# Kernel tuning notes

Measured on AMD Instinct MI355X. Metric: run time of the kernel, lower is better.

The kernel has to match this reference:

```python
import jax, jax.numpy as jnp
import numpy as np

N, E, B = 20000, 320000, 64
H, D = 4, 64          # heads, out_channels per head
HD = H * D            # 256
F_IN = 4
NUM_ACTIONS = 100
NEG_SLOPE = 0.2


def _lin(k, fan_in, fan_out, scale=0.05):
    kw, kb = jax.random.split(k)
    return (jax.random.normal(kw, (fan_in, fan_out), jnp.float32) * scale,
            jax.random.normal(kb, (fan_out,), jnp.float32) * scale)


def setup_inputs() -> dict:
    key = jax.random.key(0)
    ks = jax.random.split(key, 32)
    x = jax.random.normal(ks[0], (N, F_IN), jnp.float32)
    edge_index = jax.random.randint(ks[1], (2, E), 0, N)
    edge_attr = jax.random.normal(ks[2], (E, 1), jnp.float32)
    batch_idx = jnp.sort(jax.random.randint(ks[3], (N,), 0, B))
    action = jax.random.randint(ks[4], (B,), 0, NUM_ACTIONS)

    # GATv2 layer 1 (in=4)
    Wl1, bl1 = _lin(ks[5], F_IN, HD)
    Wr1, br1 = _lin(ks[6], F_IN, HD)
    We1 = jax.random.normal(ks[7], (1, HD), jnp.float32) * 0.05
    att1 = jax.random.normal(ks[8], (H, D), jnp.float32) * 0.05
    b1 = jnp.zeros((HD,), jnp.float32)
    # GATv2 layer 2 (in=256)
    Wl2, bl2 = _lin(ks[9], HD, HD)
    Wr2, br2 = _lin(ks[10], HD, HD)
    We2 = jax.random.normal(ks[11], (1, HD), jnp.float32) * 0.05
    att2 = jax.random.normal(ks[12], (H, D), jnp.float32) * 0.05
    b2 = jnp.zeros((HD,), jnp.float32)
    # critic MLP 256->128->64->1
    Wc1, bc1 = _lin(ks[13], 256, 128)
    Wc2, bc2 = _lin(ks[14], 128, 64)
    Wc3, bc3 = _lin(ks[15], 64, 1)
    # actor MLP 256->128->64->num_actions
    Wa1, ba1 = _lin(ks[16], 256, 128)
    Wa2, ba2 = _lin(ks[17], 128, 64)
    Wa3, ba3 = _lin(ks[18], 64, NUM_ACTIONS)
    return dict(x=x, edge_index=edge_index, edge_attr=edge_attr, batch_idx=batch_idx,
                action=action,
                Wl1=Wl1, bl1=bl1, Wr1=Wr1, br1=br1, We1=We1, att1=att1, b1=b1,
                Wl2=Wl2, bl2=bl2, Wr2=Wr2, br2=br2, We2=We2, att2=att2, b2=b2,
                Wc1=Wc1, bc1=bc1, Wc2=Wc2, bc2=bc2, Wc3=Wc3, bc3=bc3,
                Wa1=Wa1, ba1=ba1, Wa2=Wa2, ba2=ba2, Wa3=Wa3, ba3=ba3)


def gatv2(x, src, dst, edge_attr, Wl, bl, Wr, br, We, att, bias):
    n = x.shape[0]
    xl = (x @ Wl + bl).reshape(n, H, D)   # source transform (messages)
    xr = (x @ Wr + br).reshape(n, H, D)   # target transform
    e = (edge_attr @ We).reshape(-1, H, D)
    m = xl[src] + xr[dst] + e             # [E,H,D]
    s = jnp.sum(jax.nn.leaky_relu(m, NEG_SLOPE) * att, axis=-1)  # [E,H]
    smax = jax.ops.segment_max(s, dst, num_segments=n)
    a = jnp.exp(s - smax[dst])
    denom = jax.ops.segment_sum(a, dst, num_segments=n)
    alpha = a / (denom[dst] + 1e-16)      # scatter-softmax over in-edges
    out = jax.ops.segment_sum(alpha[..., None] * xl[src], dst, num_segments=n)
    return out.reshape(n, HD) + bias


def mlp3(f, W1, b1, W2, b2, W3, b3):
    h = jax.nn.relu(f @ W1 + b1)
    h = jax.nn.relu(h @ W2 + b2)
    return h @ W3 + b3


def reference(x, edge_index, edge_attr, batch_idx, action,
              Wl1, bl1, Wr1, br1, We1, att1, b1,
              Wl2, bl2, Wr2, br2, We2, att2, b2,
              Wc1, bc1, Wc2, bc2, Wc3, bc3,
              Wa1, ba1, Wa2, ba2, Wa3, ba3):
    src, dst = edge_index[0], edge_index[1]
    h = jax.nn.relu(gatv2(x, src, dst, edge_attr, Wl1, bl1, Wr1, br1, We1, att1, b1))
    h = jax.nn.relu(gatv2(h, src, dst, edge_attr, Wl2, bl2, Wr2, br2, We2, att2, b2))
    # global mean pool over graphs
    sums = jax.ops.segment_sum(h, batch_idx, num_segments=B)
    cnts = jax.ops.segment_sum(jnp.ones((h.shape[0],), h.dtype), batch_idx, num_segments=B)
    feats = sums / jnp.maximum(cnts, 1.0)[:, None]          # [B,256]
    logits = mlp3(feats, Wa1, ba1, Wa2, ba2, Wa3, ba3)       # [B,A]
    value = mlp3(feats, Wc1, bc1, Wc2, bc2, Wc3, bc3)        # [B,1]
    logp = jax.nn.log_softmax(logits, axis=-1)
    log_prob = jnp.take_along_axis(logp, action[:, None], axis=-1)[:, 0]
    entropy = -jnp.sum(jnp.exp(logp) * logp, axis=-1)
    return logits, log_prob, entropy, value
```

## Files before the change

### kernel.cpp

```cpp
#include <hip/hip_runtime.h>
#include <hip/hip_bf16.h>
#include <cstddef>

typedef __hip_bfloat16 bf16;
typedef unsigned short u16;
typedef __attribute__((ext_vector_type(8))) short short8;
typedef __attribute__((ext_vector_type(4))) float float4v;
typedef __attribute__((ext_vector_type(2))) float float2v;

#define HD 256
#define A_MAX 128

static __device__ __forceinline__ float b2f(const bf16 v) { return __bfloat162float(v); }
static __device__ __forceinline__ bf16 f2b(float v) { return __float2bfloat16(v); }

static __device__ __forceinline__ float2v up2(unsigned int u) {
  union { unsigned int i; float f; } a, b;
  a.i = u << 16; b.i = u & 0xffff0000u;
  float2v r; r.x = a.f; r.y = b.f; return r;
}

static __device__ __forceinline__ float ldf(const void* p, size_t i, bool f32) {
  return f32 ? ((const float*)p)[i] : b2f(((const bf16*)p)[i]);
}
template <bool F32>
static __device__ __forceinline__ float ldt(const void* p, size_t i) {
  return F32 ? ((const float*)p)[i] : b2f(((const bf16*)p)[i]);
}
static __device__ __forceinline__ void stf(void* p, size_t i, bool f32, float v) {
  if (f32) ((float*)p)[i] = v;
  else     ((bf16*)p)[i] = f2b(v);
}

__global__ void k_sentinel(float* out, int n, float v) {
  int i = blockIdx.x * blockDim.x + threadIdx.x;
  if (i < n) out[i] = v;
}

__global__ void k_init(const u16* __restrict__ xbits, int* __restrict__ flag,
                       int* deg, int N) {
  int i = blockIdx.x * blockDim.x + threadIdx.x;
  if (blockIdx.x == 0 && threadIdx.x < 64) {
    int l = threadIdx.x;
    int huge = 0;
    for (int k = l; k < 256; k += 64) {
      u16 u = xbits[2 * k];
      int ex = (u >> 7) & 0xFF;
      if (ex >= 0xB0) huge++;
    }
#pragma unroll
    for (int off = 32; off > 0; off >>= 1) huge += __shfl_xor(huge, off, 64);
    if (l == 0) *flag = (huge >= 20) ? 1 : 0;
  }
  if (i < N) deg[i] = 0;
}


__global__ void k_hist(const int* __restrict__ dst, int* __restrict__ deg, int E) {
  int e = blockIdx.x * blockDim.x + threadIdx.x;
  if (e < E) atomicAdd(&deg[dst[e]], 1);
}

__global__ void k_sumb(const int* __restrict__ deg, int* __restrict__ bsum, int n) {
  __shared__ int ws[16];
  int b = blockIdx.x, t = threadIdx.x;
  int i = b * 1024 + t;
  int v = (i < n) ? deg[i] : 0;
#pragma unroll
  for (int off = 32; off > 0; off >>= 1) v += __shfl_xor(v, off, 64);
  if ((t & 63) == 0) ws[t >> 6] = v;
  __syncthreads();
  if (t == 0) {
    int s = 0;
#pragma unroll
    for (int k = 0; k < 16; k++) s += ws[k];
    bsum[b] = s;
  }
}

__global__ void k_scanb(const int* __restrict__ bsum, int* __restrict__ boff,
                        int nb, int* __restrict__ offs, int n) {
  if (threadIdx.x == 0) {
    int s = 0;
    for (int i = 0; i < nb; i++) { boff[i] = s; s += bsum[i]; }
    offs[n] = s;
  }
}

__global__ void k_scanapply(const int* __restrict__ deg, const int* __restrict__ boff,
                            int* __restrict__ offs, int n) {
  __shared__ int wsum[16];
  int b = blockIdx.x, t = threadIdx.x, w = t >> 6, l = t & 63;
  int i = b * 1024 + t;
  int v = (i < n) ? deg[i] : 0;
  int x = v;
#pragma unroll
  for (int off = 1; off < 64; off <<= 1) {
    int y = __shfl_up(x, off, 64);
    if (l >= off) x += y;
  }
  if (l == 63) wsum[w] = x;
  __syncthreads();
  if (t == 0) {
    int s = 0;
#pragma unroll
    for (int k = 0; k < 16; k++) { int tmp = wsum[k]; wsum[k] = s; s += tmp; }
  }
  __syncthreads();
  if (i < n) offs[i] = boff[b] + wsum[w] + x - v;
}

__global__ void k_scatter(const int* __restrict__ src, const int* __restrict__ dst,
                          const void* __restrict__ ea, int* __restrict__ offs,
                          int2* __restrict__ csr, const int* __restrict__ flag, int E) {
  int e = blockIdx.x * blockDim.x + threadIdx.x;
  if (e >= E) return;
  bool f32 = flag[0] != 0;
  int d = dst[e];
  int pos = atomicAdd(&offs[d], 1);
  int2 v;
  v.x = src[e];
  v.y = __float_as_int(ldf(ea, e, f32));
  csr[pos] = v;
}


template <bool F32>
static __device__ void xform1_body(const void* __restrict__ x,
                                   const void* __restrict__ Wl, const void* __restrict__ bl,
                                   const void* __restrict__ Wr, const void* __restrict__ br,
                                   bf16* __restrict__ xl, bf16* __restrict__ xr, int N) {
  int n0 = blockIdx.x * 4, t = threadIdx.x;
  float wl0 = ldt<F32>(Wl, t),          wl1 = ldt<F32>(Wl, HD + t);
  float wl2 = ldt<F32>(Wl, 2 * HD + t), wl3 = ldt<F32>(Wl, 3 * HD + t);
  float wr0 = ldt<F32>(Wr, t),          wr1 = ldt<F32>(Wr, HD + t);
  float wr2 = ldt<F32>(Wr, 2 * HD + t), wr3 = ldt<F32>(Wr, 3 * HD + t);
  float bbl = ldt<F32>(bl, t), bbr = ldt<F32>(br, t);
#pragma unroll
  for (int k = 0; k < 4; k++) {
    int n = n0 + k;
    if (n >= N) break;
    float x0 = ldt<F32>(x, (size_t)n * 4 + 0), x1 = ldt<F32>(x, (size_t)n * 4 + 1);
    float x2 = ldt<F32>(x, (size_t)n * 4 + 2), x3 = ldt<F32>(x, (size_t)n * 4 + 3);
    xl[(size_t)n * HD + t] = f2b(bbl + x0 * wl0 + x1 * wl1 + x2 * wl2 + x3 * wl3);
    xr[(size_t)n * HD + t] = f2b(bbr + x0 * wr0 + x1 * wr1 + x2 * wr2 + x3 * wr3);
  }
}

__global__ void k_xform1(const void* __restrict__ x,
                         const void* __restrict__ Wl, const void* __restrict__ bl,
                         const void* __restrict__ Wr, const void* __restrict__ br,
                         bf16* __restrict__ xl, bf16* __restrict__ xr,
                         const int* __restrict__ flag, int N) {
  if (flag[0] != 0) xform1_body<true >(x, Wl, bl, Wr, br, xl, xr, N);
  else              xform1_body<false>(x, Wl, bl, Wr, br, xl, xr, N);
}

__global__ void k_prepw(const void* __restrict__ Wl, const void* __restrict__ Wr,
                        const void* __restrict__ bl, const void* __restrict__ br,
                        bf16* __restrict__ Wfrag, bf16* __restrict__ bias2,
                        const int* __restrict__ flag) {
  bool f32 = flag[0] != 0;
  int b = blockIdx.x;
  int ct = b >> 3, kt = b & 7;
  int t = threadIdx.x;
  if (b == 0) {
    bias2[t]       = f2b(ldf(bl, t, f32));
    bias2[t + 256] = f2b(ldf(br, t, f32));
  }
#pragma unroll
  for (int half = 0; half < 2; half++) {
    int e = half * 256 + t;
    int m = e & 15;
    int rest = e >> 4;
    int quad = rest >> 3, j = rest & 7;
    int l = quad * 16 + m;
    int k = kt * 32 + quad * 8 + j;
    int n = ct * 16 + m;
    const void* W = (n < 256) ? Wl : Wr;
    float v = ldf(W, (size_t)k * 256 + (n & 255), f32);
    Wfrag[(size_t)b * 512 + l * 8 + j] = f2b(v);
  }
}

__global__ __launch_bounds__(256) void k_xform2_mfma(
    const bf16* __restrict__ hin, const bf16* __restrict__ Wfrag,
    const bf16* __restrict__ bias2,
    bf16* __restrict__ P, bf16* __restrict__ Q, int N) {
  int w = threadIdx.x >> 6, l = threadIdx.x & 63;
  int r0 = blockIdx.x * 16;
  if (r0 >= N) return;
  int m = l & 15;
  int quad = l >> 4;
  int row = r0 + m;
  if (row >= N) row = N - 1;

  short8 a[8];
  const u16* arow = (const u16*)hin + (size_t)row * 256;
#pragma unroll
  for (int kt = 0; kt < 8; kt++)
    a[kt] = *(const short8*)(arow + kt * 32 + quad * 8);

#pragma unroll
  for (int ct = 0; ct < 8; ct++) {
    int c_tile = w * 8 + ct;
    int c = c_tile * 16 + m;
    const u16* bbase = (const u16*)Wfrag + ((size_t)c_tile * 8) * 512 + l * 8;
    float4v acc = {0.f, 0.f, 0.f, 0.f};
#pragma unroll
    for (int kt = 0; kt < 8; kt++) {
      short8 b = *(const short8*)(bbase + kt * 512);
      acc = __builtin_amdgcn_mfma_f32_16x16x32_bf16(a[kt], b, acc, 0, 0, 0);
    }
    float bv = b2f(bias2[c]);
#pragma unroll
    for (int i = 0; i < 4; i++) {
      int r = r0 + quad * 4 + i;
      if (r < N) {
        float v = acc[i] + bv;
        if (c < 256) P[(size_t)r * 256 + c] = f2b(v);
        else         Q[(size_t)r * 256 + (c - 256)] = f2b(v);
      }
    }
  }
}

__global__ __launch_bounds__(256) void k_gat(
    const bf16* __restrict__ xl, const bf16* __restrict__ xr,
    const int2* __restrict__ csr, const int* __restrict__ offs,
    const void* __restrict__ We, const void* __restrict__ att,
    const void* __restrict__ bias,
    bf16* __restrict__ hout, const int* __restrict__ flag, int N) {
  int w = threadIdx.x >> 6, l = threadIdx.x & 63;
  int n = blockIdx.x * 4 + w;
  if (n >= N) return;
  bool f32 = flag[0] != 0;
  int d0 = l << 2;

  uint2 xu = *(const uint2*)((const u16*)xr + (size_t)n * HD + d0);
  float2v xr01 = up2(xu.x), xr23 = up2(xu.y);
  float2v We01, We23, at01, at23;
  We01.x = ldf(We, d0 + 0, f32); We01.y = ldf(We, d0 + 1, f32);
  We23.x = ldf(We, d0 + 2, f32); We23.y = ldf(We, d0 + 3, f32);
  at01.x = ldf(att, d0 + 0, f32); at01.y = ldf(att, d0 + 1, f32);
  at23.x = ldf(att, d0 + 2, f32); at23.y = ldf(att, d0 + 3, f32);

  int beg = (n > 0) ? offs[n - 1] : 0;
  int end = offs[n];
  float2v acc01 = {0.f, 0.f}, acc23 = {0.f, 0.f};
  float dn = 0.f;

  int j = beg;
  for (; j + 2 <= end; j += 2) {
    int2 v0 = csr[j];
    int2 v1 = csr[j + 1];
    uint2 su0 = *(const uint2*)((const u16*)xl + (size_t)v0.x * HD + d0);
    uint2 su1 = *(const uint2*)((const u16*)xl + (size_t)v1.x * HD + d0);
    float ea0 = __int_as_float(v0.y), ea1 = __int_as_float(v1.y);
    float2v x01a = up2(su0.x), x23a = up2(su0.y);
    float2v x01b = up2(su1.x), x23b = up2(su1.y);
    float2v eva; eva.x = ea0; eva.y = ea0;
    float2v evb; evb.x = ea1; evb.y = ea1;
    float2v m01a = x01a + xr01 + eva * We01, m23a = x23a + xr23 + eva * We23;
    float2v m01b = x01b + xr01 + evb * We01, m23b = x23b + xr23 + evb * We23;
    float2v lr01a, lr23a, lr01b, lr23b;
    lr01a.x = fmaxf(m01a.x, 0.2f * m01a.x); lr01a.y = fmaxf(m01a.y, 0.2f * m01a.y);
    lr23a.x = fmaxf(m23a.x, 0.2f * m23a.x); lr23a.y = fmaxf(m23a.y, 0.2f * m23a.y);
    lr01b.x = fmaxf(m01b.x, 0.2f * m01b.x); lr01b.y = fmaxf(m01b.y, 0.2f * m01b.y);
    lr23b.x = fmaxf(m23b.x, 0.2f * m23b.x); lr23b.y = fmaxf(m23b.y, 0.2f * m23b.y);
    float2v ppa = lr01a * at01 + lr23a * at23;
    float2v ppb = lr01b * at01 + lr23b * at23;
    float psa = ppa.x + ppa.y;
    float psb = ppb.x + ppb.y;
    psa += __shfl_xor(psa, 1, 64);  psb += __shfl_xor(psb, 1, 64);
    psa += __shfl_xor(psa, 2, 64);  psb += __shfl_xor(psb, 2, 64);
    psa += __shfl_xor(psa, 4, 64);  psb += __shfl_xor(psb, 4, 64);
    psa += __shfl_xor(psa, 8, 64);  psb += __shfl_xor(psb, 8, 64);
    float aa = __expf(fminf(fmaxf(psa, -40.f), 40.f));
    float ab = __expf(fminf(fmaxf(psb, -40.f), 40.f));
    dn += aa + ab;
    float2v ava; ava.x = aa; ava.y = aa;
    float2v avb; avb.x = ab; avb.y = ab;
    acc01 += ava * x01a + avb * x01b;
    acc23 += ava * x23a + avb * x23b;
  }
  if (j < end) {
    int2 v = csr[j];
    float eav = __int_as_float(v.y);
    uint2 su = *(const uint2*)((const u16*)xl + (size_t)v.x * HD + d0);
    float2v x01 = up2(su.x), x23 = up2(su.y);
    float2v ev; ev.x = eav; ev.y = eav;
    float2v m01 = x01 + xr01 + ev * We01;
    float2v m23 = x23 + xr23 + ev * We23;
    float2v lr01, lr23;
    lr01.x = fmaxf(m01.x, 0.2f * m01.x); lr01.y = fmaxf(m01.y, 0.2f * m01.y);
    lr23.x = fmaxf(m23.x, 0.2f * m23.x); lr23.y = fmaxf(m23.y, 0.2f * m23.y);
    float2v pp = lr01 * at01 + lr23 * at23;
    float ps = pp.x + pp.y;
    ps += __shfl_xor(ps, 1, 64);
    ps += __shfl_xor(ps, 2, 64);
    ps += __shfl_xor(ps, 4, 64);
    ps += __shfl_xor(ps, 8, 64);
    float a = __expf(fminf(fmaxf(ps, -40.f), 40.f));
    dn += a;
    float2v av; av.x = a; av.y = a;
    acc01 += av * x01;
    acc23 += av * x23;
  }

  float inv = 1.f / (dn + 1e-16f);
  bf16 o[4];
  o[0] = f2b(fmaxf(acc01.x * inv + ldf(bias, d0 + 0, f32), 0.f));
  o[1] = f2b(fmaxf(acc01.y * inv + ldf(bias, d0 + 1, f32), 0.f));
  o[2] = f2b(fmaxf(acc23.x * inv + ldf(bias, d0 + 2, f32), 0.f));
  o[3] = f2b(fmaxf(acc23.y * inv + ldf(bias, d0 + 3, f32), 0.f));
  *(ushort4*)((u16*)hout + (size_t)n * HD + d0) = *(ushort4*)o;
}


static __device__ __forceinline__ int lb(const int* a, int n, int v) {
  int lo = 0, hi = n;
  while (lo < hi) { int m = (lo + hi) >> 1; if (a[m] < v) lo = m + 1; else hi = m; }
  return lo;
}

__global__ void k_pool(const bf16* __restrict__ h, const int* __restrict__ bidx,
                       float* __restrict__ feats4, int Bc, int N) {
  int g = blockIdx.x >> 2, part = blockIdx.x & 3, t = threadIdx.x;
  int s = lb(bidx, N, g), e_ = lb(bidx, N, g + 1);
  float acc = 0.f;
  for (int i = s + part; i < e_; i += 4) acc += b2f(h[(size_t)i * HD + t]);
  feats4[((size_t)part * Bc + g) * HD + t] = acc;
}


template <bool F32>
static __device__ void mlp_body(const float* __restrict__ feats4,
                                const int* __restrict__ bidx, int N,
                                const int* __restrict__ act,
                                const void* Wa1, const void* ba1, const void* Wa2, const void* ba2,
                                const void* Wa3, const void* ba3,
                                const void* Wc1, const void* bc1, const void* Wc2, const void* bc2,
                                const void* Wc3, const void* bc3,
                                void* __restrict__ out, int B, int A) {
  __shared__ float f[HD];
  __shared__ float p1[2][128];
  __shared__ float h1[128];
  __shared__ float p2[4][64];
  __shared__ float h2[64];
  __shared__ float lg[A_MAX];
  __shared__ float sc[2];
  __shared__ float inv_s;
  int blk = blockIdx.x, g = blk >> 1, which = blk & 1, t = threadIdx.x;
  if (t == 0) {
    int cnt = lb(bidx, N, g + 1) - lb(bidx, N, g);
    inv_s = 1.f / fmaxf((float)cnt, 1.f);
  }
  __syncthreads();
  float inv = inv_s;
  f[t] = (feats4[(size_t)g * HD + t] + feats4[((size_t)B + g) * HD + t]
        + feats4[((size_t)2 * B + g) * HD + t] + feats4[((size_t)3 * B + g) * HD + t]) * inv;
  __syncthreads();

  const void *W1 = which ? Wc1 : Wa1, *B1 = which ? bc1 : ba1;
  const void *W2 = which ? Wc2 : Wa2, *B2 = which ? bc2 : ba2;

  {
    int j = t & 127, half = t >> 7;
    int i0 = half * 128;
    float a0 = 0.f, a1 = 0.f, a2 = 0.f, a3 = 0.f;
    for (int u = 0; u < 128; u += 4) {
      a0 += f[i0 + u + 0] * ldt<F32>(W1, (size_t)(i0 + u + 0) * 128 + j);
      a1 += f[i0 + u + 1] * ldt<F32>(W1, (size_t)(i0 + u + 1) * 128 + j);
      a2 += f[i0 + u + 2] * ldt<F32>(W1, (size_t)(i0 + u + 2) * 128 + j);
      a3 += f[i0 + u + 3] * ldt<F32>(W1, (size_t)(i0 + u + 3) * 128 + j);
    }
    p1[half][j] = (a0 + a1) + (a2 + a3);
  }
  __syncthreads();
  if (t < 128) h1[t] = fmaxf(p1[0][t] + p1[1][t] + ldt<F32>(B1, t), 0.f);
  __syncthreads();

  {
    int j = t & 63, q = t >> 6;
    int i0 = q * 32;
    float a0 = 0.f, a1 = 0.f;
    for (int u = 0; u < 32; u += 2) {
      a0 += h1[i0 + u + 0] * ldt<F32>(W2, (size_t)(i0 + u + 0) * 64 + j);
      a1 += h1[i0 + u + 1] * ldt<F32>(W2, (size_t)(i0 + u + 1) * 64 + j);
    }
    p2[q][j] = a0 + a1;
  }
  __syncthreads();
  if (t < 64) h2[t] = fmaxf(p2[0][t] + p2[1][t] + p2[2][t] + p2[3][t] + ldt<F32>(B2, t), 0.f);
  __syncthreads();

  if (which == 0) {
    if (t < A) {
      float a0 = 0.f, a1 = 0.f, a2 = 0.f, a3 = 0.f;
      for (int i = 0; i < 64; i += 4) {
        a0 += h2[i + 0] * ldt<F32>(Wa3, (size_t)(i + 0) * A + t);
        a1 += h2[i + 1] * ldt<F32>(Wa3, (size_t)(i + 1) * A + t);
        a2 += h2[i + 2] * ldt<F32>(Wa3, (size_t)(i + 2) * A + t);
        a3 += h2[i + 3] * ldt<F32>(Wa3, (size_t)(i + 3) * A + t);
      }
      lg[t] = (a0 + a1) + (a2 + a3) + ldt<F32>(ba3, t);
    }
    __syncthreads();
    if (t == 0) {
      float mx = -3.4e38f;
      for (int i = 0; i < A; i++) mx = fmaxf(mx, lg[i]);
      float s = 0.f;
      for (int i = 0; i < A; i++) s += __expf(lg[i] - mx);
      sc[0] = mx;
      sc[1] = logf(s);
    }
    __syncthreads();
    float mx = sc[0], lse = sc[1];
    if (t < A) stf(out, (size_t)g * A + t, F32, lg[t]);
    if (t == 0) {
      int a = act[g];
      stf(out, (size_t)B * A + g, F32, lg[a] - mx - lse);
      float ent = 0.f;
      for (int i = 0; i < A; i++) {
        float l = lg[i] - mx - lse;
        ent -= __expf(l) * l;
      }
      stf(out, (size_t)B * A + B + g, F32, ent);
    }
  } else {
    if (t < 64) {
      float v = h2[t] * ldt<F32>(Wc3, t);
#pragma unroll
      for (int off = 32; off > 0; off >>= 1) v += __shfl_xor(v, off, 64);
      if (t == 0) stf(out, (size_t)B * A + 2 * B + g, F32, v + ldt<F32>(bc3, 0));
    }
  }
}

__global__ void k_mlp(const float* __restrict__ feats4,
                      const int* __restrict__ bidx, int N,
                      const int* __restrict__ act,
                      const void* Wa1, const void* ba1, const void* Wa2, const void* ba2,
                      const void* Wa3, const void* ba3,
                      const void* Wc1, const void* bc1, const void* Wc2, const void* bc2,
                      const void* Wc3, const void* bc3,
                      void* __restrict__ out, const int* __restrict__ flag, int B, int A) {
  if (flag[0] != 0)
    mlp_body<true >(feats4, bidx, N, act, Wa1, ba1, Wa2, ba2, Wa3, ba3,
                    Wc1, bc1, Wc2, bc2, Wc3, bc3, out, B, A);
  else
    mlp_body<false>(feats4, bidx, N, act, Wa1, ba1, Wa2, ba2, Wa3, ba3,
                    Wc1, bc1, Wc2, bc2, Wc3, bc3, out, B, A);
}


extern "C" void kernel_launch(void* const* d_in, const int* in_sizes, int n_in,
                              void* d_out, int out_size, void* d_ws, size_t ws_size,
                              hipStream_t stream) {
  const void* x    = d_in[0];
  const int*  ei   = (const int*)d_in[1];
  const void* ea   = d_in[2];
  const int*  bidx = (const int*)d_in[3];
  const int*  act  = (const int*)d_in[4];
  const void *Wl1 = d_in[5],  *bl1 = d_in[6];
  const void *Wr1 = d_in[7],  *br1 = d_in[8];
  const void *We1 = d_in[9],  *att1 = d_in[10];
  const void *b1  = d_in[11];
  const void *Wl2 = d_in[12], *bl2 = d_in[13];
  const void *Wr2 = d_in[14], *br2 = d_in[15];
  const void *We2 = d_in[16], *att2 = d_in[17];
  const void *b2  = d_in[18];
  const void *Wc1 = d_in[19], *bc1 = d_in[20];
  const void *Wc2 = d_in[21], *bc2 = d_in[22];
  const void *Wc3 = d_in[23], *bc3 = d_in[24];
  const void *Wa1 = d_in[25], *ba1 = d_in[26];
  const void *Wa2 = d_in[27], *ba2 = d_in[28];
  const void *Wa3 = d_in[29], *ba3 = d_in[30];

  const int N = in_sizes[0] / 4;
  const int E = in_sizes[1] / 2;
  const int B = in_sizes[4];
  const int A = in_sizes[30];

  char* p = (char*)d_ws;
  auto carve = [&](size_t bytes) {
    void* r = (void*)p;
    p += (bytes + 255) & ~(size_t)255;
    return r;
  };
  int*   dflag   = (int*)carve(4);
  int*   deg     = (int*)carve((size_t)N * 4);
  int*   offs    = (int*)carve((size_t)(N + 1) * 4);
  int2*  csr     = (int2*)carve((size_t)E * 8);
  bf16*  P       = (bf16*)carve((size_t)N * HD * 2);
  bf16*  Q       = (bf16*)carve((size_t)N * HD * 2);
  bf16*  R       = (bf16*)carve((size_t)N * HD * 2);
  bf16*  Wfrag   = (bf16*)carve((size_t)512 * 256 * 2);
  bf16*  bias2   = (bf16*)carve((size_t)512 * 2);
  float* feats4  = (float*)carve((size_t)4 * B * HD * 4);
  int    nb      = (N + 1023) / 1024;
  int*   bsum    = (int*)carve((size_t)nb * 4);
  int*   boff    = (int*)carve((size_t)nb * 4);
  size_t need = (size_t)(p - (char*)d_ws);

  if (ws_size < need) {
    float v = 1000.f + (float)(ws_size >> 20);
    int n = out_size / 2;
    k_sentinel<<<(n + 255) / 256, 256, 0, stream>>>((float*)d_out, n, v);
    return;
  }

  const int* srcA = ei;
  const int* dstA = ei + E;

  k_init<<<(N + 255) / 256, 256, 0, stream>>>((const u16*)x, dflag, deg, N);
  k_hist<<<(E + 255) / 256, 256, 0, stream>>>(dstA, deg, E);
  k_sumb<<<nb, 1024, 0, stream>>>(deg, bsum, N);
  k_scanb<<<1, 64, 0, stream>>>(bsum, boff, nb, offs, N);
  k_scanapply<<<nb, 1024, 0, stream>>>(deg, boff, offs, N);
  k_scatter<<<(E + 255) / 256, 256, 0, stream>>>(srcA, dstA, ea, offs, csr, dflag, E);
  k_prepw<<<256, 256, 0, stream>>>(Wl2, Wr2, bl2, br2, Wfrag, bias2, dflag);

  k_xform1<<<(N + 3) / 4, 256, 0, stream>>>(x, Wl1, bl1, Wr1, br1, P, Q, dflag, N);
  k_gat<<<(N + 3) / 4, 256, 0, stream>>>(P, Q, csr, offs, We1, att1, b1, R, dflag, N);
  k_xform2_mfma<<<(N + 15) / 16, 256, 0, stream>>>(R, Wfrag, bias2, P, Q, N);
  k_gat<<<(N + 3) / 4, 256, 0, stream>>>(P, Q, csr, offs, We2, att2, b2, R, dflag, N);

  k_pool<<<B * 4, 256, 0, stream>>>(R, bidx, feats4, B, N);
  k_mlp<<<B * 2, 256, 0, stream>>>(feats4, bidx, N, act,
                                   Wa1, ba1, Wa2, ba2, Wa3, ba3,
                                   Wc1, bc1, Wc2, bc2, Wc3, bc3,
                                   d_out, dflag, B, A);
}
```

Baseline: 318.2 us.

## Merge scan, scatter, xform1, prepw launches; unroll GAT edges by four; fuse pooling into MLP

Replaces the three-kernel prefix scan with a single-block looped scan and merges the CSR scatter, layer-1 transform and weight-fragment prep into one multi-role launch. The GAT edge loop is unrolled to process four edges at once, with batched shuffle reductions for more loads in flight. Mean pooling moves into the MLP kernel, removing the pool launch and its feats buffer. In exchange, each MLP block reads its graph's rows serially, and the actor and critic blocks duplicate that read.

```diff
diff --git a/kernel.cpp b/kernel.cpp
--- a/kernel.cpp
+++ b/kernel.cpp
@@ -55,131 +55,103 @@
   if (i < N) deg[i] = 0;
 }
 
-
 __global__ void k_hist(const int* __restrict__ dst, int* __restrict__ deg, int E) {
   int e = blockIdx.x * blockDim.x + threadIdx.x;
   if (e < E) atomicAdd(&deg[dst[e]], 1);
 }
 
-__global__ void k_sumb(const int* __restrict__ deg, int* __restrict__ bsum, int n) {
-  __shared__ int ws[16];
+__global__ void k_scan(const int* __restrict__ deg, int* __restrict__ offs, int n) {
+  __shared__ int wsum[17];
+  __shared__ int carry_s;
+  int t = threadIdx.x, w = t >> 6, l = t & 63;
+  if (t == 0) carry_s = 0;
+  __syncthreads();
+  for (int base = 0; base < n; base += 1024) {
+    int i = base + t;
+    int v = (i < n) ? deg[i] : 0;
+    int x = v;
+#pragma unroll
+    for (int off = 1; off < 64; off <<= 1) {
+      int y = __shfl_up(x, off, 64);
+      if (l >= off) x += y;
+    }
+    if (l == 63) wsum[w] = x;
+    __syncthreads();
+    if (t == 0) {
+      int s = 0;
+#pragma unroll
+      for (int k = 0; k < 16; k++) { int tmp = wsum[k]; wsum[k] = s; s += tmp; }
+      wsum[16] = s;
+    }
+    __syncthreads();
+    int c = carry_s;
+    if (i < n) offs[i] = c + wsum[w] + x - v;
+    __syncthreads();
+    if (t == 0) carry_s = c + wsum[16];
+    __syncthreads();
+  }
+  if (t == 0) offs[n] = carry_s;
+}
+
+__global__ void k_misc(const int* __restrict__ src, const int* __restrict__ dst,
+                       const void* __restrict__ ea, int* __restrict__ offs,
+                       int2* __restrict__ csr,
+                       const void* __restrict__ x,
+                       const void* __restrict__ Wl1, const void* __restrict__ bl1,
+                       const void* __restrict__ Wr1, const void* __restrict__ br1,
+                       bf16* __restrict__ P, bf16* __restrict__ Q,
+                       const void* __restrict__ Wl2, const void* __restrict__ Wr2,
+                       const void* __restrict__ bl2, const void* __restrict__ br2,
+                       bf16* __restrict__ Wfrag, bf16* __restrict__ bias2,
+                       const int* __restrict__ flag,
+                       int E, int N, int nSc, int nX1) {
+  bool f32 = flag[0] != 0;
   int b = blockIdx.x, t = threadIdx.x;
-  int i = b * 1024 + t;
-  int v = (i < n) ? deg[i] : 0;
-#pragma unroll
-  for (int off = 32; off > 0; off >>= 1) v += __shfl_xor(v, off, 64);
-  if ((t & 63) == 0) ws[t >> 6] = v;
-  __syncthreads();
-  if (t == 0) {
-    int s = 0;
-#pragma unroll
-    for (int k = 0; k < 16; k++) s += ws[k];
-    bsum[b] = s;
-  }
-}
-
-__global__ void k_scanb(const int* __restrict__ bsum, int* __restrict__ boff,
-                        int nb, int* __restrict__ offs, int n) {
-  if (threadIdx.x == 0) {
-    int s = 0;
-    for (int i = 0; i < nb; i++) { boff[i] = s; s += bsum[i]; }
-    offs[n] = s;
-  }
-}
-
-__global__ void k_scanapply(const int* __restrict__ deg, const int* __restrict__ boff,
-                            int* __restrict__ offs, int n) {
-  __shared__ int wsum[16];
-  int b = blockIdx.x, t = threadIdx.x, w = t >> 6, l = t & 63;
-  int i = b * 1024 + t;
-  int v = (i < n) ? deg[i] : 0;
-  int x = v;
-#pragma unroll
-  for (int off = 1; off < 64; off <<= 1) {
-    int y = __shfl_up(x, off, 64);
-    if (l >= off) x += y;
-  }
-  if (l == 63) wsum[w] = x;
-  __syncthreads();
-  if (t == 0) {
-    int s = 0;
-#pragma unroll
-    for (int k = 0; k < 16; k++) { int tmp = wsum[k]; wsum[k] = s; s += tmp; }
-  }
-  __syncthreads();
-  if (i < n) offs[i] = boff[b] + wsum[w] + x - v;
-}
-
-__global__ void k_scatter(const int* __restrict__ src, const int* __restrict__ dst,
-                          const void* __restrict__ ea, int* __restrict__ offs,
-                          int2* __restrict__ csr, const int* __restrict__ flag, int E) {
-  int e = blockIdx.x * blockDim.x + threadIdx.x;
-  if (e >= E) return;
-  bool f32 = flag[0] != 0;
-  int d = dst[e];
-  int pos = atomicAdd(&offs[d], 1);
-  int2 v;
-  v.x = src[e];
-  v.y = __float_as_int(ldf(ea, e, f32));
-  csr[pos] = v;
-}
-
-
-template <bool F32>
-static __device__ void xform1_body(const void* __restrict__ x,
-                                   const void* __restrict__ Wl, const void* __restrict__ bl,
-                                   const void* __restrict__ Wr, const void* __restrict__ br,
-                                   bf16* __restrict__ xl, bf16* __restrict__ xr, int N) {
-  int n0 = blockIdx.x * 4, t = threadIdx.x;
-  float wl0 = ldt<F32>(Wl, t),          wl1 = ldt<F32>(Wl, HD + t);
-  float wl2 = ldt<F32>(Wl, 2 * HD + t), wl3 = ldt<F32>(Wl, 3 * HD + t);
-  float wr0 = ldt<F32>(Wr, t),          wr1 = ldt<F32>(Wr, HD + t);
-  float wr2 = ldt<F32>(Wr, 2 * HD + t), wr3 = ldt<F32>(Wr, 3 * HD + t);
-  float bbl = ldt<F32>(bl, t), bbr = ldt<F32>(br, t);
-#pragma unroll
-  for (int k = 0; k < 4; k++) {
-    int n = n0 + k;
-    if (n >= N) break;
-    float x0 = ldt<F32>(x, (size_t)n * 4 + 0), x1 = ldt<F32>(x, (size_t)n * 4 + 1);
-    float x2 = ldt<F32>(x, (size_t)n * 4 + 2), x3 = ldt<F32>(x, (size_t)n * 4 + 3);
-    xl[(size_t)n * HD + t] = f2b(bbl + x0 * wl0 + x1 * wl1 + x2 * wl2 + x3 * wl3);
-    xr[(size_t)n * HD + t] = f2b(bbr + x0 * wr0 + x1 * wr1 + x2 * wr2 + x3 * wr3);
-  }
-}
-
-__global__ void k_xform1(const void* __restrict__ x,
-                         const void* __restrict__ Wl, const void* __restrict__ bl,
-                         const void* __restrict__ Wr, const void* __restrict__ br,
-                         bf16* __restrict__ xl, bf16* __restrict__ xr,
-                         const int* __restrict__ flag, int N) {
-  if (flag[0] != 0) xform1_body<true >(x, Wl, bl, Wr, br, xl, xr, N);
-  else              xform1_body<false>(x, Wl, bl, Wr, br, xl, xr, N);
-}
-
-__global__ void k_prepw(const void* __restrict__ Wl, const void* __restrict__ Wr,
-                        const void* __restrict__ bl, const void* __restrict__ br,
-                        bf16* __restrict__ Wfrag, bf16* __restrict__ bias2,
-                        const int* __restrict__ flag) {
-  bool f32 = flag[0] != 0;
-  int b = blockIdx.x;
-  int ct = b >> 3, kt = b & 7;
-  int t = threadIdx.x;
-  if (b == 0) {
-    bias2[t]       = f2b(ldf(bl, t, f32));
-    bias2[t + 256] = f2b(ldf(br, t, f32));
-  }
-#pragma unroll
-  for (int half = 0; half < 2; half++) {
-    int e = half * 256 + t;
-    int m = e & 15;
-    int rest = e >> 4;
-    int quad = rest >> 3, j = rest & 7;
-    int l = quad * 16 + m;
-    int k = kt * 32 + quad * 8 + j;
-    int n = ct * 16 + m;
-    const void* W = (n < 256) ? Wl : Wr;
-    float v = ldf(W, (size_t)k * 256 + (n & 255), f32);
-    Wfrag[(size_t)b * 512 + l * 8 + j] = f2b(v);
+  if (b < nSc) {
+    int e = b * 256 + t;
+    if (e >= E) return;
+    int d = dst[e];
+    int pos = atomicAdd(&offs[d], 1);
+    int2 v;
+    v.x = src[e];
+    v.y = __float_as_int(ldf(ea, e, f32));
+    csr[pos] = v;
+  } else if (b < nSc + nX1) {
+    int n0 = (b - nSc) * 4;
+    float wl0 = ldf(Wl1, t, f32),          wl1 = ldf(Wl1, HD + t, f32);
+    float wl2 = ldf(Wl1, 2 * HD + t, f32), wl3 = ldf(Wl1, 3 * HD + t, f32);
+    float wr0 = ldf(Wr1, t, f32),          wr1 = ldf(Wr1, HD + t, f32);
+    float wr2 = ldf(Wr1, 2 * HD + t, f32), wr3 = ldf(Wr1, 3 * HD + t, f32);
+    float bbl = ldf(bl1, t, f32), bbr = ldf(br1, t, f32);
+#pragma unroll
+    for (int k = 0; k < 4; k++) {
+      int n = n0 + k;
+      if (n >= N) break;
+      float x0 = ldf(x, (size_t)n * 4 + 0, f32), x1 = ldf(x, (size_t)n * 4 + 1, f32);
+      float x2 = ldf(x, (size_t)n * 4 + 2, f32), x3 = ldf(x, (size_t)n * 4 + 3, f32);
+      P[(size_t)n * HD + t] = f2b(bbl + x0 * wl0 + x1 * wl1 + x2 * wl2 + x3 * wl3);
+      Q[(size_t)n * HD + t] = f2b(bbr + x0 * wr0 + x1 * wr1 + x2 * wr2 + x3 * wr3);
+    }
+  } else {
+    int pb = b - nSc - nX1;
+    int ct = pb >> 3, kt = pb & 7;
+    if (pb == 0) {
+      bias2[t]       = f2b(ldf(bl2, t, f32));
+      bias2[t + 256] = f2b(ldf(br2, t, f32));
+    }
+#pragma unroll
+    for (int half = 0; half < 2; half++) {
+      int e = half * 256 + t;
+      int m = e & 15;
+      int rest = e >> 4;
+      int quad = rest >> 3, j = rest & 7;
+      int l = quad * 16 + m;
+      int k = kt * 32 + quad * 8 + j;
+      int n = ct * 16 + m;
+      const void* W = (n < 256) ? Wl2 : Wr2;
+      float v = ldf(W, (size_t)k * 256 + (n & 255), f32);
+      Wfrag[(size_t)pb * 512 + l * 8 + j] = f2b(v);
+    }
   }
 }
 
@@ -251,40 +223,44 @@
   float dn = 0.f;
 
   int j = beg;
-  for (; j + 2 <= end; j += 2) {
-    int2 v0 = csr[j];
-    int2 v1 = csr[j + 1];
-    uint2 su0 = *(const uint2*)((const u16*)xl + (size_t)v0.x * HD + d0);
-    uint2 su1 = *(const uint2*)((const u16*)xl + (size_t)v1.x * HD + d0);
-    float ea0 = __int_as_float(v0.y), ea1 = __int_as_float(v1.y);
-    float2v x01a = up2(su0.x), x23a = up2(su0.y);
-    float2v x01b = up2(su1.x), x23b = up2(su1.y);
-    float2v eva; eva.x = ea0; eva.y = ea0;
-    float2v evb; evb.x = ea1; evb.y = ea1;
-    float2v m01a = x01a + xr01 + eva * We01, m23a = x23a + xr23 + eva * We23;
-    float2v m01b = x01b + xr01 + evb * We01, m23b = x23b + xr23 + evb * We23;
-    float2v lr01a, lr23a, lr01b, lr23b;
-    lr01a.x = fmaxf(m01a.x, 0.2f * m01a.x); lr01a.y = fmaxf(m01a.y, 0.2f * m01a.y);
-    lr23a.x = fmaxf(m23a.x, 0.2f * m23a.x); lr23a.y = fmaxf(m23a.y, 0.2f * m23a.y);
-    lr01b.x = fmaxf(m01b.x, 0.2f * m01b.x); lr01b.y = fmaxf(m01b.y, 0.2f * m01b.y);
-    lr23b.x = fmaxf(m23b.x, 0.2f * m23b.x); lr23b.y = fmaxf(m23b.y, 0.2f * m23b.y);
-    float2v ppa = lr01a * at01 + lr23a * at23;
-    float2v ppb = lr01b * at01 + lr23b * at23;
-    float psa = ppa.x + ppa.y;
-    float psb = ppb.x + ppb.y;
-    psa += __shfl_xor(psa, 1, 64);  psb += __shfl_xor(psb, 1, 64);
-    psa += __shfl_xor(psa, 2, 64);  psb += __shfl_xor(psb, 2, 64);
-    psa += __shfl_xor(psa, 4, 64);  psb += __shfl_xor(psb, 4, 64);
-    psa += __shfl_xor(psa, 8, 64);  psb += __shfl_xor(psb, 8, 64);
-    float aa = __expf(fminf(fmaxf(psa, -40.f), 40.f));
-    float ab = __expf(fminf(fmaxf(psb, -40.f), 40.f));
-    dn += aa + ab;
-    float2v ava; ava.x = aa; ava.y = aa;
-    float2v avb; avb.x = ab; avb.y = ab;
-    acc01 += ava * x01a + avb * x01b;
-    acc23 += ava * x23a + avb * x23b;
-  }
-  if (j < end) {
+  for (; j + 4 <= end; j += 4) {
+    int2 v[4];
+#pragma unroll
+    for (int q = 0; q < 4; q++) v[q] = csr[j + q];
+    uint2 su[4];
+#pragma unroll
+    for (int q = 0; q < 4; q++)
+      su[q] = *(const uint2*)((const u16*)xl + (size_t)v[q].x * HD + d0);
+    float2v x01[4], x23[4];
+    float ps[4];
+#pragma unroll
+    for (int q = 0; q < 4; q++) {
+      x01[q] = up2(su[q].x); x23[q] = up2(su[q].y);
+      float eav = __int_as_float(v[q].y);
+      float2v ev; ev.x = eav; ev.y = eav;
+      float2v m01 = x01[q] + xr01 + ev * We01;
+      float2v m23 = x23[q] + xr23 + ev * We23;
+      float2v lr01, lr23;
+      lr01.x = fmaxf(m01.x, 0.2f * m01.x); lr01.y = fmaxf(m01.y, 0.2f * m01.y);
+      lr23.x = fmaxf(m23.x, 0.2f * m23.x); lr23.y = fmaxf(m23.y, 0.2f * m23.y);
+      float2v pp = lr01 * at01 + lr23 * at23;
+      ps[q] = pp.x + pp.y;
+    }
+#pragma unroll
+    for (int off = 1; off <= 8; off <<= 1) {
+#pragma unroll
+      for (int q = 0; q < 4; q++) ps[q] += __shfl_xor(ps[q], off, 64);
+    }
+#pragma unroll
+    for (int q = 0; q < 4; q++) {
+      float a = __expf(fminf(fmaxf(ps[q], -40.f), 40.f));
+      dn += a;
+      float2v av; av.x = a; av.y = a;
+      acc01 += av * x01[q];
+      acc23 += av * x23[q];
+    }
+  }
+  for (; j < end; j++) {
     int2 v = csr[j];
     float eav = __int_as_float(v.y);
     uint2 su = *(const uint2*)((const u16*)xl + (size_t)v.x * HD + d0);
@@ -324,18 +300,8 @@
   return lo;
 }
 
-__global__ void k_pool(const bf16* __restrict__ h, const int* __restrict__ bidx,
-                       float* __restrict__ feats4, int Bc, int N) {
-  int g = blockIdx.x >> 2, part = blockIdx.x & 3, t = threadIdx.x;
-  int s = lb(bidx, N, g), e_ = lb(bidx, N, g + 1);
-  float acc = 0.f;
-  for (int i = s + part; i < e_; i += 4) acc += b2f(h[(size_t)i * HD + t]);
-  feats4[((size_t)part * Bc + g) * HD + t] = acc;
-}
-
-
 template <bool F32>
-static __device__ void mlp_body(const float* __restrict__ feats4,
+static __device__ void mlp_body(const bf16* __restrict__ R,
                                 const int* __restrict__ bidx, int N,
                                 const int* __restrict__ act,
                                 const void* Wa1, const void* ba1, const void* Wa2, const void* ba2,
@@ -350,16 +316,21 @@
   __shared__ float h2[64];
   __shared__ float lg[A_MAX];
   __shared__ float sc[2];
-  __shared__ float inv_s;
   int blk = blockIdx.x, g = blk >> 1, which = blk & 1, t = threadIdx.x;
-  if (t == 0) {
-    int cnt = lb(bidx, N, g + 1) - lb(bidx, N, g);
-    inv_s = 1.f / fmaxf((float)cnt, 1.f);
-  }
-  __syncthreads();
-  float inv = inv_s;
-  f[t] = (feats4[(size_t)g * HD + t] + feats4[((size_t)B + g) * HD + t]
-        + feats4[((size_t)2 * B + g) * HD + t] + feats4[((size_t)3 * B + g) * HD + t]) * inv;
+  int s_ = lb(bidx, N, g), e_ = lb(bidx, N, g + 1);
+  float inv = 1.f / fmaxf((float)(e_ - s_), 1.f);
+  {
+    float a0 = 0.f, a1 = 0.f, a2 = 0.f, a3 = 0.f;
+    int i = s_;
+    for (; i + 4 <= e_; i += 4) {
+      a0 += b2f(R[(size_t)(i + 0) * HD + t]);
+      a1 += b2f(R[(size_t)(i + 1) * HD + t]);
+      a2 += b2f(R[(size_t)(i + 2) * HD + t]);
+      a3 += b2f(R[(size_t)(i + 3) * HD + t]);
+    }
+    for (; i < e_; i++) a0 += b2f(R[(size_t)i * HD + t]);
+    f[t] = ((a0 + a1) + (a2 + a3)) * inv;
+  }
   __syncthreads();
 
   const void *W1 = which ? Wc1 : Wa1, *B1 = which ? bc1 : ba1;
@@ -438,7 +409,7 @@
   }
 }
 
-__global__ void k_mlp(const float* __restrict__ feats4,
+__global__ void k_mlp(const bf16* __restrict__ R,
                       const int* __restrict__ bidx, int N,
                       const int* __restrict__ act,
                       const void* Wa1, const void* ba1, const void* Wa2, const void* ba2,
@@ -447,10 +418,10 @@
                       const void* Wc3, const void* bc3,
                       void* __restrict__ out, const int* __restrict__ flag, int B, int A) {
   if (flag[0] != 0)
-    mlp_body<true >(feats4, bidx, N, act, Wa1, ba1, Wa2, ba2, Wa3, ba3,
+    mlp_body<true >(R, bidx, N, act, Wa1, ba1, Wa2, ba2, Wa3, ba3,
                     Wc1, bc1, Wc2, bc2, Wc3, bc3, out, B, A);
   else
-    mlp_body<false>(feats4, bidx, N, act, Wa1, ba1, Wa2, ba2, Wa3, ba3,
+    mlp_body<false>(R, bidx, N, act, Wa1, ba1, Wa2, ba2, Wa3, ba3,
                     Wc1, bc1, Wc2, bc2, Wc3, bc3, out, B, A);
 }
 
@@ -498,10 +469,6 @@
   bf16*  R       = (bf16*)carve((size_t)N * HD * 2);
   bf16*  Wfrag   = (bf16*)carve((size_t)512 * 256 * 2);
   bf16*  bias2   = (bf16*)carve((size_t)512 * 2);
-  float* feats4  = (float*)carve((size_t)4 * B * HD * 4);
-  int    nb      = (N + 1023) / 1024;
-  int*   bsum    = (int*)carve((size_t)nb * 4);
-  int*   boff    = (int*)carve((size_t)nb * 4);
   size_t need = (size_t)(p - (char*)d_ws);
 
   if (ws_size < need) {
@@ -514,21 +481,20 @@
   const int* srcA = ei;
   const int* dstA = ei + E;
 
+  int nSc = (E + 255) / 256;
+  int nX1 = (N + 3) / 4;
+
   k_init<<<(N + 255) / 256, 256, 0, stream>>>((const u16*)x, dflag, deg, N);
   k_hist<<<(E + 255) / 256, 256, 0, stream>>>(dstA, deg, E);
-  k_sumb<<<nb, 1024, 0, stream>>>(deg, bsum, N);
-  k_scanb<<<1, 64, 0, stream>>>(bsum, boff, nb, offs, N);
-  k_scanapply<<<nb, 1024, 0, stream>>>(deg, boff, offs, N);
-  k_scatter<<<(E + 255) / 256, 256, 0, stream>>>(srcA, dstA, ea, offs, csr, dflag, E);
-  k_prepw<<<256, 256, 0, stream>>>(Wl2, Wr2, bl2, br2, Wfrag, bias2, dflag);
-
-  k_xform1<<<(N + 3) / 4, 256, 0, stream>>>(x, Wl1, bl1, Wr1, br1, P, Q, dflag, N);
+  k_scan<<<1, 1024, 0, stream>>>(deg, offs, N);
+  k_misc<<<nSc + nX1 + 256, 256, 0, stream>>>(srcA, dstA, ea, offs, csr,
+                                              x, Wl1, bl1, Wr1, br1, P, Q,
+                                              Wl2, Wr2, bl2, br2, Wfrag, bias2,
+                                              dflag, E, N, nSc, nX1);
   k_gat<<<(N + 3) / 4, 256, 0, stream>>>(P, Q, csr, offs, We1, att1, b1, R, dflag, N);
   k_xform2_mfma<<<(N + 15) / 16, 256, 0, stream>>>(R, Wfrag, bias2, P, Q, N);
   k_gat<<<(N + 3) / 4, 256, 0, stream>>>(P, Q, csr, offs, We2, att2, b2, R, dflag, N);
-
-  k_pool<<<B * 4, 256, 0, stream>>>(R, bidx, feats4, B, N);
-  k_mlp<<<B * 2, 256, 0, stream>>>(feats4, bidx, N, act,
+  k_mlp<<<B * 2, 256, 0, stream>>>(R, bidx, N, act,
                                    Wa1, ba1, Wa2, ba2, Wa3, ba3,
                                    Wc1, bc1, Wc2, bc2, Wc3, bc3,
                                    d_out, dflag, B, A);
```

New measurement: 318.8 us. No clear change (+0.2%).
